# Performance work log

Measured on AMD Instinct MI355X. Metric: run time of the kernel, lower is better.

## Reference

```python
import jax, jax.numpy as jnp
import numpy as np

N_NODES = 10000
N_EDGES = 320000
HIDDEN = 256
HEADS = 8
HEAD_DIM = HIDDEN // HEADS  # 32
NEG_SLOPE = 0.2


def setup_inputs() -> dict:
    key = jax.random.key(0)
    ks = jax.random.split(key, 12)
    x = jax.random.normal(ks[0], (N_NODES, HIDDEN), dtype=jnp.float32)
    edges_idx = jax.random.randint(ks[1], (2, N_EDGES), 0, N_NODES, dtype=jnp.int64)
    s = 1.0 / np.sqrt(HIDDEN)
    # layer 1 params
    W1 = jax.random.normal(ks[2], (HIDDEN, HEADS * HEAD_DIM), dtype=jnp.float32) * s
    a_src1 = jax.random.normal(ks[3], (HEADS, HEAD_DIM), dtype=jnp.float32) * s
    a_dst1 = jax.random.normal(ks[4], (HEADS, HEAD_DIM), dtype=jnp.float32) * s
    b1 = jnp.zeros((HEADS * HEAD_DIM,), dtype=jnp.float32)
    # layer 2 params
    W2 = jax.random.normal(ks[5], (HIDDEN, HEADS * HEAD_DIM), dtype=jnp.float32) * s
    a_src2 = jax.random.normal(ks[6], (HEADS, HEAD_DIM), dtype=jnp.float32) * s
    a_dst2 = jax.random.normal(ks[7], (HEADS, HEAD_DIM), dtype=jnp.float32) * s
    b2 = jnp.zeros((HEADS * HEAD_DIM,), dtype=jnp.float32)
    return {"x": x, "edges_idx": edges_idx,
            "W1": W1, "a_src1": a_src1, "a_dst1": a_dst1, "b1": b1,
            "W2": W2, "a_src2": a_src2, "a_dst2": a_dst2, "b2": b2}


def gat_conv(x, src, dst, W, a_src, a_dst, b):
    """PyG GATConv (concat=True, negative_slope=0.2), dropout in eval mode."""
    N = x.shape[0]
    h = (x @ W).reshape(N, HEADS, HEAD_DIM)          # [N,H,C]
    alpha_s = jnp.einsum('nhc,hc->nh', h, a_src)     # [N,H]
    alpha_d = jnp.einsum('nhc,hc->nh', h, a_dst)     # [N,H]
    e = alpha_s[src] + alpha_d[dst]                  # [E,H]
    e = jnp.where(e > 0, e, NEG_SLOPE * e)           # leaky_relu
    # scatter-softmax over incoming edges of each dst node
    m = jax.ops.segment_max(e, dst, num_segments=N)  # [N,H]
    ex = jnp.exp(e - m[dst])                         # [E,H]
    denom = jax.ops.segment_sum(ex, dst, num_segments=N)  # [N,H]
    alpha = ex / (denom[dst] + 1e-16)                # [E,H]
    msg = h[src] * alpha[:, :, None]                 # [E,H,C]
    out = jax.ops.segment_sum(msg, dst, num_segments=N)   # [N,H,C]
    return out.reshape(N, HEADS * HEAD_DIM) + b


def reference(x, edges_idx, W1, a_src1, a_dst1, b1, W2, a_src2, a_dst2, b2):
    src = edges_idx[0]
    dst = edges_idx[1]
    h = gat_conv(x, src, dst, W1, a_src1, a_dst1, b1)
    h = jax.nn.elu(h)
    out = gat_conv(h, src, dst, W2, a_src2, a_dst2, b2)
    return out
```

## Files before the change

### kernel.cpp

```cpp
#include <hip/hip_runtime.h>
#include <hip/hip_bf16.h>

#define N_NODES 10000
#define N_EDGES 320000
#define HIDDEN 256
#define HEADS 8
#define HEAD_DIM 32
#define NEG_SLOPE 0.2f
#define CAP 80

typedef __attribute__((ext_vector_type(8))) short short8;
typedef __attribute__((ext_vector_type(4))) float f32x4;

__device__ __forceinline__ void bf16_split(float v, unsigned short& hi, unsigned short& lo) {
    __hip_bfloat16 hb = __float2bfloat16(v);
    float hf = __bfloat162float(hb);
    __hip_bfloat16 lb = __float2bfloat16(v - hf);
    hi = *reinterpret_cast<unsigned short*>(&hb);
    lo = *reinterpret_cast<unsigned short*>(&lb);
}

__global__ __launch_bounds__(256) void prep_kernel(
    const float* __restrict__ W1, const float* __restrict__ W2,
    const int* __restrict__ src, const int* __restrict__ dst,
    unsigned short* __restrict__ w1h, unsigned short* __restrict__ w1l,
    unsigned short* __restrict__ w2h, unsigned short* __restrict__ w2l,
    int* __restrict__ counts, int* __restrict__ csr_src) {
    int b = blockIdx.x;
    int tid = threadIdx.x;
    if (b < 512) {
        int i = b * 256 + tid;
        int which = i >> 16;
        int rem = i & 0xFFFF;
        int k = rem >> 8, n = rem & 255;
        const float* W = which ? W2 : W1;
        unsigned short* wh = which ? w2h : w1h;
        unsigned short* wl = which ? w2l : w1l;
        unsigned short h, l;
        bf16_split(W[k * 256 + n], h, l);
        wh[n * 256 + k] = h;
        wl[n * 256 + k] = l;
    } else {
        int e = (b - 512) * 256 + tid;
        int d = dst[e];
        int rank = atomicAdd(&counts[d], 1);
        csr_src[d * CAP + rank] = src[e];
    }
}

template <int AFP32>
__global__ __launch_bounds__(256) void gemm_mfma_kernel(
    const float* __restrict__ Axf,
    const unsigned short* __restrict__ Ah, const unsigned short* __restrict__ Al,
    const unsigned short* __restrict__ BhT, const unsigned short* __restrict__ BlT,
    float* __restrict__ C, const float* __restrict__ a_src,
    const float* __restrict__ a_dst, float* __restrict__ alpha_s,
    float* __restrict__ alpha_d) {
    __shared__ __align__(16) unsigned short sAh[80 * 40];
    __shared__ __align__(16) unsigned short sAl[80 * 40];
    __shared__ __align__(16) unsigned short sBh[128 * 40];
    __shared__ __align__(16) unsigned short sBl[128 * 40];
    const int tid = threadIdx.x;
    const int w = tid >> 6, lane = tid & 63;
    const int col = lane & 15, quad = lane >> 4;
    const int m0 = blockIdx.y * 80, n0 = blockIdx.x * 128;

    f32x4 acc[5][2] = {};

    float4 raf[3];
    uint4 rau[3];
    uint4 rb[4];

#define LOAD_A(k0)                                                              \
    if (AFP32) {                                                                \
        _Pragma("unroll") for (int i = 0; i < 3; ++i) {                         \
            int t = tid + i * 256;                                              \
            if (t < 640) {                                                      \
                int row = t >> 3, seg = t & 7;                                  \
                raf[i] = *(const float4*)&Axf[(size_t)(m0 + row) * 256 + (k0) + seg * 4]; \
            }                                                                   \
        }                                                                       \
    } else {                                                                    \
        _Pragma("unroll") for (int i = 0; i < 3; ++i) {                         \
            int t = tid + i * 256;                                              \
            if (t < 640) {                                                      \
                int tt = t < 320 ? t : t - 320;                                 \
                int row = tt >> 2, seg = tt & 3;                                \
                const unsigned short* P = t < 320 ? Ah : Al;                    \
                rau[i] = *(const uint4*)&P[(size_t)(m0 + row) * 256 + (k0) + seg * 8]; \
            }                                                                   \
        }                                                                       \
    }
#define LOAD_B(k0)                                                              \
    _Pragma("unroll") for (int i = 0; i < 4; ++i) {                             \
        int t = tid + i * 256;                                                  \
        int tt = t < 512 ? t : t - 512;                                         \
        int row = tt >> 2, seg = tt & 3;                                        \
        const unsigned short* P = t < 512 ? BhT : BlT;                          \
        rb[i] = *(const uint4*)&P[(size_t)(n0 + row) * 256 + (k0) + seg * 8];   \
    }

    LOAD_A(0)
    LOAD_B(0)

    for (int ks = 0; ks < 8; ++ks) {
        if (AFP32) {
#pragma unroll
            for (int i = 0; i < 3; ++i) {
                int t = tid + i * 256;
                if (t < 640) {
                    int row = t >> 3, seg = t & 7;
                    float4 v = raf[i];
                    ushort4 hh, ll;
                    unsigned short hb, lb;
                    bf16_split(v.x, hb, lb); hh.x = hb; ll.x = lb;
                    bf16_split(v.y, hb, lb); hh.y = hb; ll.y = lb;
                    bf16_split(v.z, hb, lb); hh.z = hb; ll.z = lb;
                    bf16_split(v.w, hb, lb); hh.w = hb; ll.w = lb;
                    *(ushort4*)&sAh[row * 40 + seg * 4] = hh;
                    *(ushort4*)&sAl[row * 40 + seg * 4] = ll;
                }
            }
        } else {
#pragma unroll
            for (int i = 0; i < 3; ++i) {
                int t = tid + i * 256;
                if (t < 640) {
                    int tt = t < 320 ? t : t - 320;
                    int row = tt >> 2, seg = tt & 3;
                    unsigned short* S = t < 320 ? sAh : sAl;
                    *(uint4*)&S[row * 40 + seg * 8] = rau[i];
                }
            }
        }
#pragma unroll
        for (int i = 0; i < 4; ++i) {
            int t = tid + i * 256;
            int tt = t < 512 ? t : t - 512;
            int row = tt >> 2, seg = tt & 3;
            unsigned short* S = t < 512 ? sBh : sBl;
            *(uint4*)&S[row * 40 + seg * 8] = rb[i];
        }
        __syncthreads();

        if (ks < 7) {
            int nk = (ks + 1) * 32;
            LOAD_A(nk)
            LOAD_B(nk)
        }

        short8 bh0 = *(const short8*)&sBh[(w * 32 + col) * 40 + quad * 8];
        short8 bl0 = *(const short8*)&sBl[(w * 32 + col) * 40 + quad * 8];
        short8 bh1 = *(const short8*)&sBh[(w * 32 + 16 + col) * 40 + quad * 8];
        short8 bl1 = *(const short8*)&sBl[(w * 32 + 16 + col) * 40 + quad * 8];
#pragma unroll
        for (int rt = 0; rt < 5; ++rt) {
            short8 ah = *(const short8*)&sAh[(rt * 16 + col) * 40 + quad * 8];
            short8 al = *(const short8*)&sAl[(rt * 16 + col) * 40 + quad * 8];
            acc[rt][0] = __builtin_amdgcn_mfma_f32_16x16x32_bf16(ah, bh0, acc[rt][0], 0, 0, 0);
            acc[rt][0] = __builtin_amdgcn_mfma_f32_16x16x32_bf16(ah, bl0, acc[rt][0], 0, 0, 0);
            acc[rt][0] = __builtin_amdgcn_mfma_f32_16x16x32_bf16(al, bh0, acc[rt][0], 0, 0, 0);
            acc[rt][1] = __builtin_amdgcn_mfma_f32_16x16x32_bf16(ah, bh1, acc[rt][1], 0, 0, 0);
            acc[rt][1] = __builtin_amdgcn_mfma_f32_16x16x32_bf16(ah, bl1, acc[rt][1], 0, 0, 0);
            acc[rt][1] = __builtin_amdgcn_mfma_f32_16x16x32_bf16(al, bh1, acc[rt][1], 0, 0, 0);
        }
        __syncthreads();
    }
#undef LOAD_A
#undef LOAD_B

    const int head = blockIdx.x * 4 + w;
    float as0 = a_src[n0 + w * 32 + col];
    float as1 = a_src[n0 + w * 32 + 16 + col];
    float ad0 = a_dst[n0 + w * 32 + col];
    float ad1 = a_dst[n0 + w * 32 + 16 + col];
#pragma unroll
    for (int rt = 0; rt < 5; ++rt) {
#pragma unroll
        for (int r = 0; r < 4; ++r) {
            int gm = m0 + rt * 16 + quad * 4 + r;
            C[(size_t)gm * 256 + n0 + w * 32 + col]      = acc[rt][0][r];
            C[(size_t)gm * 256 + n0 + w * 32 + 16 + col] = acc[rt][1][r];
            float ps = acc[rt][0][r] * as0 + acc[rt][1][r] * as1;
            float pd = acc[rt][0][r] * ad0 + acc[rt][1][r] * ad1;
#pragma unroll
            for (int m = 1; m < 16; m <<= 1) {
                ps += __shfl_xor(ps, m);
                pd += __shfl_xor(pd, m);
            }
            if (col == 0) {
                alpha_s[gm * HEADS + head] = ps;
                alpha_d[gm * HEADS + head] = pd;
            }
        }
    }
}

__global__ __launch_bounds__(256) void aggregate_kernel(
    const int* __restrict__ counts, const int* __restrict__ csr_src,
    const float* __restrict__ alpha_s, const float* __restrict__ alpha_d,
    const float* __restrict__ h, const float* __restrict__ bias,
    float* __restrict__ outf, unsigned short* __restrict__ oh,
    unsigned short* __restrict__ ol, int mode) {
    const int tid = threadIdx.x;
    const int w = tid >> 6, lane = tid & 63;
    const int pair = blockIdx.x / 2500;
    const int d = (blockIdx.x - pair * 2500) * 4 + w;
    const int q = lane >> 4, fl = lane & 15;
    const int hd = pair * 2 + (fl >> 3);
    const float ad = alpha_d[d * HEADS + hd];
    const int n = counts[d];
    const int* __restrict__ bucket = csr_src + d * CAP;

    const float* hp = h + pair * 64 + fl * 4;
    float4 acc = make_float4(0.f, 0.f, 0.f, 0.f);
    float den = 0.f;

    int i = q * 4;
    for (; i + 3 < n; i += 16) {
        int4 s4 = *(const int4*)&bucket[i];
        float al0 = alpha_s[s4.x * HEADS + hd];
        float al1 = alpha_s[s4.y * HEADS + hd];
        float al2 = alpha_s[s4.z * HEADS + hd];
        float al3 = alpha_s[s4.w * HEADS + hd];
        float4 h0 = *(const float4*)&hp[(size_t)s4.x * HIDDEN];
        float4 h1 = *(const float4*)&hp[(size_t)s4.y * HIDDEN];
        float4 h2 = *(const float4*)&hp[(size_t)s4.z * HIDDEN];
        float4 h3 = *(const float4*)&hp[(size_t)s4.w * HIDDEN];
        float e0 = al0 + ad; e0 = e0 > 0.f ? e0 : NEG_SLOPE * e0;
        float e1 = al1 + ad; e1 = e1 > 0.f ? e1 : NEG_SLOPE * e1;
        float e2 = al2 + ad; e2 = e2 > 0.f ? e2 : NEG_SLOPE * e2;
        float e3 = al3 + ad; e3 = e3 > 0.f ? e3 : NEG_SLOPE * e3;
        float ev0 = __expf(e0), ev1 = __expf(e1);
        float ev2 = __expf(e2), ev3 = __expf(e3);
        den += (ev0 + ev1) + (ev2 + ev3);
        acc.x += h0.x * ev0 + h1.x * ev1 + h2.x * ev2 + h3.x * ev3;
        acc.y += h0.y * ev0 + h1.y * ev1 + h2.y * ev2 + h3.y * ev3;
        acc.z += h0.z * ev0 + h1.z * ev1 + h2.z * ev2 + h3.z * ev3;
        acc.w += h0.w * ev0 + h1.w * ev1 + h2.w * ev2 + h3.w * ev3;
    }
    for (; i < n; ++i) {
        int s0 = bucket[i];
        float al0 = alpha_s[s0 * HEADS + hd];
        float4 h0 = *(const float4*)&hp[(size_t)s0 * HIDDEN];
        float e0 = al0 + ad; e0 = e0 > 0.f ? e0 : NEG_SLOPE * e0;
        float ev0 = __expf(e0);
        den += ev0;
        acc.x += h0.x * ev0; acc.y += h0.y * ev0;
        acc.z += h0.z * ev0; acc.w += h0.w * ev0;
    }

    acc.x += __shfl_xor(acc.x, 16); acc.y += __shfl_xor(acc.y, 16);
    acc.z += __shfl_xor(acc.z, 16); acc.w += __shfl_xor(acc.w, 16);
    den += __shfl_xor(den, 16);
    acc.x += __shfl_xor(acc.x, 32); acc.y += __shfl_xor(acc.y, 32);
    acc.z += __shfl_xor(acc.z, 32); acc.w += __shfl_xor(acc.w, 32);
    den += __shfl_xor(den, 32);

    if (q == 0) {
        float inv = 1.f / (den + 1e-16f);
        float4 bv = *(const float4*)&bias[pair * 64 + fl * 4];
        float v[4];
        v[0] = acc.x * inv + bv.x;
        v[1] = acc.y * inv + bv.y;
        v[2] = acc.z * inv + bv.z;
        v[3] = acc.w * inv + bv.w;
        size_t oidx = (size_t)d * HIDDEN + pair * 64 + fl * 4;
        if (mode == 1) {
            ushort4 hh, ll;
            unsigned short hb, lb;
#pragma unroll
            for (int k = 0; k < 4; ++k)
                v[k] = v[k] > 0.f ? v[k] : (__expf(v[k]) - 1.f);
            bf16_split(v[0], hb, lb); hh.x = hb; ll.x = lb;
            bf16_split(v[1], hb, lb); hh.y = hb; ll.y = lb;
            bf16_split(v[2], hb, lb); hh.z = hb; ll.z = lb;
            bf16_split(v[3], hb, lb); hh.w = hb; ll.w = lb;
            *(ushort4*)&oh[oidx] = hh;
            *(ushort4*)&ol[oidx] = ll;
        } else {
            *(float4*)&outf[oidx] = make_float4(v[0], v[1], v[2], v[3]);
        }
    }
}

extern "C" void kernel_launch(void* const* d_in, const int* in_sizes, int n_in,
                              void* d_out, int out_size, void* d_ws, size_t ws_size,
                              hipStream_t stream) {
    const float* x      = (const float*)d_in[0];
    const int*   edges  = (const int*)d_in[1];
    const float* W1     = (const float*)d_in[2];
    const float* as1    = (const float*)d_in[3];
    const float* ad1    = (const float*)d_in[4];
    const float* b1     = (const float*)d_in[5];
    const float* W2     = (const float*)d_in[6];
    const float* as2    = (const float*)d_in[7];
    const float* ad2    = (const float*)d_in[8];
    const float* b2     = (const float*)d_in[9];
    float* out = (float*)d_out;

    const int* src = edges;
    const int* dst = edges + N_EDGES;

    const size_t NF = (size_t)N_NODES * HIDDEN;
    const size_t NH = (size_t)N_NODES * HEADS;

    char* base = (char*)d_ws;
    float* h_buf = (float*)base;                base += NF * 4;
    unsigned short* x2h = (unsigned short*)base; base += NF * 2;
    unsigned short* x2l = (unsigned short*)base; base += NF * 2;
    float* alpha_s = (float*)base;              base += NH * 4;
    float* alpha_d = (float*)base;              base += NH * 4;
    unsigned short* w1h = (unsigned short*)base; base += 65536 * 2;
    unsigned short* w1l = (unsigned short*)base; base += 65536 * 2;
    unsigned short* w2h = (unsigned short*)base; base += 65536 * 2;
    unsigned short* w2l = (unsigned short*)base; base += 65536 * 2;
    int* csr_src = (int*)base;                  base += (size_t)N_NODES * CAP * 4;
    int* counts  = (int*)base;                  base += (size_t)N_NODES * 4;

    dim3 gemm_grid(2, 125);
    const int EB = (N_EDGES + 255) / 256;
    const int AGG_B = 2500 * 4;

    hipMemsetAsync(counts, 0, N_NODES * sizeof(int), stream);
    prep_kernel<<<512 + EB, 256, 0, stream>>>(W1, W2, src, dst,
                                              w1h, w1l, w2h, w2l, counts, csr_src);

    gemm_mfma_kernel<1><<<gemm_grid, 256, 0, stream>>>(
        x, nullptr, nullptr, w1h, w1l, h_buf, as1, ad1, alpha_s, alpha_d);
    aggregate_kernel<<<AGG_B, 256, 0, stream>>>(counts, csr_src, alpha_s, alpha_d,
                                                h_buf, b1, nullptr, x2h, x2l, 1);

    gemm_mfma_kernel<0><<<gemm_grid, 256, 0, stream>>>(
        nullptr, x2h, x2l, w2h, w2l, h_buf, as2, ad2, alpha_s, alpha_d);
    aggregate_kernel<<<AGG_B, 256, 0, stream>>>(counts, csr_src, alpha_s, alpha_d,
                                                h_buf, b2, out, nullptr, nullptr, 0);
}
```

Measured before the change: 211.9 us.

## Store projected features in fp16 and gather 8 halves per lane

The GEMM epilogue now writes the projected node features h as fp16 instead of fp32. The attention logits are still computed from the fp32 accumulators. The aggregation kernel gathers 16-byte half8 vectors per lane, so each lane covers 8 channels and the grid shrinks from four head-pair passes to two four-head passes. This halves the bytes of the random-access neighbor gather, which dominates aggregation, and halves the number of times each bucket and alpha_s are re-read. The cost is fp16 rounding of h, which could affect accuracy tolerance, plus more accumulator registers per thread.

```diff
diff --git a/kernel.cpp b/kernel.cpp
--- a/kernel.cpp
+++ b/kernel.cpp
@@ -1,5 +1,6 @@
 #include <hip/hip_runtime.h>
 #include <hip/hip_bf16.h>
+#include <hip/hip_fp16.h>
 
 #define N_NODES 10000
 #define N_EDGES 320000
@@ -10,6 +11,7 @@
 #define CAP 80
 
 typedef __attribute__((ext_vector_type(8))) short short8;
+typedef __attribute__((ext_vector_type(8))) _Float16 half8;
 typedef __attribute__((ext_vector_type(4))) float f32x4;
 
 __device__ __forceinline__ void bf16_split(float v, unsigned short& hi, unsigned short& lo) {
@@ -53,7 +55,7 @@
     const float* __restrict__ Axf,
     const unsigned short* __restrict__ Ah, const unsigned short* __restrict__ Al,
     const unsigned short* __restrict__ BhT, const unsigned short* __restrict__ BlT,
-    float* __restrict__ C, const float* __restrict__ a_src,
+    _Float16* __restrict__ hH, const float* __restrict__ a_src,
     const float* __restrict__ a_dst, float* __restrict__ alpha_s,
     float* __restrict__ alpha_d) {
     __shared__ __align__(16) unsigned short sAh[80 * 40];
@@ -179,8 +181,8 @@
 #pragma unroll
         for (int r = 0; r < 4; ++r) {
             int gm = m0 + rt * 16 + quad * 4 + r;
-            C[(size_t)gm * 256 + n0 + w * 32 + col]      = acc[rt][0][r];
-            C[(size_t)gm * 256 + n0 + w * 32 + 16 + col] = acc[rt][1][r];
+            hH[(size_t)gm * 256 + n0 + w * 32 + col]      = (_Float16)acc[rt][0][r];
+            hH[(size_t)gm * 256 + n0 + w * 32 + 16 + col] = (_Float16)acc[rt][1][r];
             float ps = acc[rt][0][r] * as0 + acc[rt][1][r] * as1;
             float pd = acc[rt][0][r] * ad0 + acc[rt][1][r] * ad1;
 #pragma unroll
@@ -199,21 +201,21 @@
 __global__ __launch_bounds__(256) void aggregate_kernel(
     const int* __restrict__ counts, const int* __restrict__ csr_src,
     const float* __restrict__ alpha_s, const float* __restrict__ alpha_d,
-    const float* __restrict__ h, const float* __restrict__ bias,
+    const _Float16* __restrict__ hH, const float* __restrict__ bias,
     float* __restrict__ outf, unsigned short* __restrict__ oh,
     unsigned short* __restrict__ ol, int mode) {
     const int tid = threadIdx.x;
     const int w = tid >> 6, lane = tid & 63;
-    const int pair = blockIdx.x / 2500;
-    const int d = (blockIdx.x - pair * 2500) * 4 + w;
+    const int ph = blockIdx.x / 2500;
+    const int d = (blockIdx.x - ph * 2500) * 4 + w;
     const int q = lane >> 4, fl = lane & 15;
-    const int hd = pair * 2 + (fl >> 3);
+    const int hd = ph * 4 + (fl >> 2);
     const float ad = alpha_d[d * HEADS + hd];
     const int n = counts[d];
     const int* __restrict__ bucket = csr_src + d * CAP;
 
-    const float* hp = h + pair * 64 + fl * 4;
-    float4 acc = make_float4(0.f, 0.f, 0.f, 0.f);
+    const _Float16* hp = hH + ph * 128 + fl * 8;
+    float acc[8] = {};
     float den = 0.f;
 
     int i = q * 4;
@@ -223,10 +225,10 @@
         float al1 = alpha_s[s4.y * HEADS + hd];
         float al2 = alpha_s[s4.z * HEADS + hd];
         float al3 = alpha_s[s4.w * HEADS + hd];
-        float4 h0 = *(const float4*)&hp[(size_t)s4.x * HIDDEN];
-        float4 h1 = *(const float4*)&hp[(size_t)s4.y * HIDDEN];
-        float4 h2 = *(const float4*)&hp[(size_t)s4.z * HIDDEN];
-        float4 h3 = *(const float4*)&hp[(size_t)s4.w * HIDDEN];
+        half8 h0 = *(const half8*)&hp[(size_t)s4.x * HIDDEN];
+        half8 h1 = *(const half8*)&hp[(size_t)s4.y * HIDDEN];
+        half8 h2 = *(const half8*)&hp[(size_t)s4.z * HIDDEN];
+        half8 h3 = *(const half8*)&hp[(size_t)s4.w * HIDDEN];
         float e0 = al0 + ad; e0 = e0 > 0.f ? e0 : NEG_SLOPE * e0;
         float e1 = al1 + ad; e1 = e1 > 0.f ? e1 : NEG_SLOPE * e1;
         float e2 = al2 + ad; e2 = e2 > 0.f ? e2 : NEG_SLOPE * e2;
@@ -234,52 +236,50 @@
         float ev0 = __expf(e0), ev1 = __expf(e1);
         float ev2 = __expf(e2), ev3 = __expf(e3);
         den += (ev0 + ev1) + (ev2 + ev3);
-        acc.x += h0.x * ev0 + h1.x * ev1 + h2.x * ev2 + h3.x * ev3;
-        acc.y += h0.y * ev0 + h1.y * ev1 + h2.y * ev2 + h3.y * ev3;
-        acc.z += h0.z * ev0 + h1.z * ev1 + h2.z * ev2 + h3.z * ev3;
-        acc.w += h0.w * ev0 + h1.w * ev1 + h2.w * ev2 + h3.w * ev3;
+#pragma unroll
+        for (int j = 0; j < 8; ++j)
+            acc[j] += (float)h0[j] * ev0 + (float)h1[j] * ev1 +
+                      (float)h2[j] * ev2 + (float)h3[j] * ev3;
     }
     for (; i < n; ++i) {
         int s0 = bucket[i];
         float al0 = alpha_s[s0 * HEADS + hd];
-        float4 h0 = *(const float4*)&hp[(size_t)s0 * HIDDEN];
+        half8 h0 = *(const half8*)&hp[(size_t)s0 * HIDDEN];
         float e0 = al0 + ad; e0 = e0 > 0.f ? e0 : NEG_SLOPE * e0;
         float ev0 = __expf(e0);
         den += ev0;
-        acc.x += h0.x * ev0; acc.y += h0.y * ev0;
-        acc.z += h0.z * ev0; acc.w += h0.w * ev0;
-    }
-
-    acc.x += __shfl_xor(acc.x, 16); acc.y += __shfl_xor(acc.y, 16);
-    acc.z += __shfl_xor(acc.z, 16); acc.w += __shfl_xor(acc.w, 16);
+#pragma unroll
+        for (int j = 0; j < 8; ++j) acc[j] += (float)h0[j] * ev0;
+    }
+
+#pragma unroll
+    for (int j = 0; j < 8; ++j) acc[j] += __shfl_xor(acc[j], 16);
     den += __shfl_xor(den, 16);
-    acc.x += __shfl_xor(acc.x, 32); acc.y += __shfl_xor(acc.y, 32);
-    acc.z += __shfl_xor(acc.z, 32); acc.w += __shfl_xor(acc.w, 32);
+#pragma unroll
+    for (int j = 0; j < 8; ++j) acc[j] += __shfl_xor(acc[j], 32);
     den += __shfl_xor(den, 32);
 
     if (q == 0) {
         float inv = 1.f / (den + 1e-16f);
-        float4 bv = *(const float4*)&bias[pair * 64 + fl * 4];
-        float v[4];
-        v[0] = acc.x * inv + bv.x;
-        v[1] = acc.y * inv + bv.y;
-        v[2] = acc.z * inv + bv.z;
-        v[3] = acc.w * inv + bv.w;
-        size_t oidx = (size_t)d * HIDDEN + pair * 64 + fl * 4;
+        float v[8];
+#pragma unroll
+        for (int j = 0; j < 8; ++j)
+            v[j] = acc[j] * inv + bias[ph * 128 + fl * 8 + j];
+        size_t oidx = (size_t)d * HIDDEN + ph * 128 + fl * 8;
         if (mode == 1) {
-            ushort4 hh, ll;
-            unsigned short hb, lb;
-#pragma unroll
-            for (int k = 0; k < 4; ++k)
-                v[k] = v[k] > 0.f ? v[k] : (__expf(v[k]) - 1.f);
-            bf16_split(v[0], hb, lb); hh.x = hb; ll.x = lb;
-            bf16_split(v[1], hb, lb); hh.y = hb; ll.y = lb;
-            bf16_split(v[2], hb, lb); hh.z = hb; ll.z = lb;
-            bf16_split(v[3], hb, lb); hh.w = hb; ll.w = lb;
-            *(ushort4*)&oh[oidx] = hh;
-            *(ushort4*)&ol[oidx] = ll;
+            unsigned short hb[8], lb[8];
+#pragma unroll
+            for (int j = 0; j < 8; ++j) {
+                v[j] = v[j] > 0.f ? v[j] : (__expf(v[j]) - 1.f);
+                bf16_split(v[j], hb[j], lb[j]);
+            }
+            *(ushort4*)&oh[oidx]     = make_ushort4(hb[0], hb[1], hb[2], hb[3]);
+            *(ushort4*)&oh[oidx + 4] = make_ushort4(hb[4], hb[5], hb[6], hb[7]);
+            *(ushort4*)&ol[oidx]     = make_ushort4(lb[0], lb[1], lb[2], lb[3]);
+            *(ushort4*)&ol[oidx + 4] = make_ushort4(lb[4], lb[5], lb[6], lb[7]);
         } else {
-            *(float4*)&outf[oidx] = make_float4(v[0], v[1], v[2], v[3]);
+            *(float4*)&outf[oidx]     = make_float4(v[0], v[1], v[2], v[3]);
+            *(float4*)&outf[oidx + 4] = make_float4(v[4], v[5], v[6], v[7]);
         }
     }
 }
@@ -306,7 +306,7 @@
     const size_t NH = (size_t)N_NODES * HEADS;
 
     char* base = (char*)d_ws;
-    float* h_buf = (float*)base;                base += NF * 4;
+    _Float16* hH = (_Float16*)base;             base += NF * 2;
     unsigned short* x2h = (unsigned short*)base; base += NF * 2;
     unsigned short* x2l = (unsigned short*)base; base += NF * 2;
     float* alpha_s = (float*)base;              base += NH * 4;
@@ -320,19 +320,19 @@
 
     dim3 gemm_grid(2, 125);
     const int EB = (N_EDGES + 255) / 256;
-    const int AGG_B = 2500 * 4;
+    const int AGG_B = 2500 * 2;
 
     hipMemsetAsync(counts, 0, N_NODES * sizeof(int), stream);
     prep_kernel<<<512 + EB, 256, 0, stream>>>(W1, W2, src, dst,
                                               w1h, w1l, w2h, w2l, counts, csr_src);
 
     gemm_mfma_kernel<1><<<gemm_grid, 256, 0, stream>>>(
-        x, nullptr, nullptr, w1h, w1l, h_buf, as1, ad1, alpha_s, alpha_d);
+        x, nullptr, nullptr, w1h, w1l, hH, as1, ad1, alpha_s, alpha_d);
     aggregate_kernel<<<AGG_B, 256, 0, stream>>>(counts, csr_src, alpha_s, alpha_d,
-                                                h_buf, b1, nullptr, x2h, x2l, 1);
+                                                hH, b1, nullptr, x2h, x2l, 1);
 
     gemm_mfma_kernel<0><<<gemm_grid, 256, 0, stream>>>(
-        nullptr, x2h, x2l, w2h, w2l, h_buf, as2, ad2, alpha_s, alpha_d);
+        nullptr, x2h, x2l, w2h, w2l, hH, as2, ad2, alpha_s, alpha_d);
     aggregate_kernel<<<AGG_B, 256, 0, stream>>>(counts, csr_src, alpha_s, alpha_d,
-                                                h_buf, b2, out, nullptr, nullptr, 0);
-}
+                                                hH, b2, out, nullptr, nullptr, 0);
+}
```

Result: faster. 194.0 us (-8.4%).
